# Optimization experiments

Measured on AMD Instinct MI355X. Metric: run time of the kernel, lower is better.

## Reference

```python
import jax, jax.numpy as jnp
import numpy as np

B, N, H, T = 2048, 512, 20, 3

def setup_inputs() -> dict:
    key = jax.random.key(0)
    ks = jax.random.split(key, 10)
    x = jax.random.normal(ks[0], (B, N, H), dtype=jnp.float32)
    # row-stochastic-ish adjacency so time-step iteration stays numerically tame
    A_in = jax.random.uniform(ks[1], (N, N), dtype=jnp.float32) / N
    std = 0.05
    W3w = jax.random.normal(ks[2], (H, 2 * H), dtype=jnp.float32) * std
    W3u = jax.random.normal(ks[3], (H, H), dtype=jnp.float32) * std
    W4w = jax.random.normal(ks[4], (H, 2 * H), dtype=jnp.float32) * std
    W4u = jax.random.normal(ks[5], (H, H), dtype=jnp.float32) * std
    W5w = jax.random.normal(ks[6], (H, 2 * H), dtype=jnp.float32) * std
    W5u = jax.random.normal(ks[7], (H, H), dtype=jnp.float32) * std
    W_out = jax.random.normal(ks[8], (H, 2 * H), dtype=jnp.float32) * std
    b_out = jnp.zeros((H,), dtype=jnp.float32)
    return {"x": x, "A_in": A_in, "W3w": W3w, "W3u": W3u, "W4w": W4w,
            "W4u": W4u, "W5w": W5w, "W5u": W5u, "W_out": W_out, "b_out": b_out}

def reference(x, A_in, W3w, W3u, W4w, W4u, W5w, W5u, W_out, b_out):
    # x: [B, N, H]; A_in: [N, N]; out-matrix is the transpose of in-matrix.
    A_out = A_in.T
    b, n, h = x.shape
    x_flat = x.reshape(b * n, h)              # original 'input' kept for skip-cat
    nodes = x                                  # batch_aog_nodes [B, N, H]
    outputs = []
    for _ in range(T):
        # aggregation: in- and out-neighborhood bmm, then concat -> [B*N, 2H]
        agg_in = jnp.einsum('nm,bmh->bnh', A_in, nodes)
        agg_out = jnp.einsum('nm,bmh->bnh', A_out, nodes)
        av = jnp.concatenate([agg_in, agg_out], axis=-1).reshape(b * n, 2 * h)
        fn = nodes.reshape(b * n, h)
        # GRU-style gates
        zv = jax.nn.sigmoid(av @ W3w.T + fn @ W3u.T)
        rv = jax.nn.sigmoid(av @ W4w.T + fn @ W4u.T)
        hv = jnp.tanh(av @ W5w.T + (rv * fn) @ W5u.T)
        fn = (1.0 - zv) * fn + zv * hv
        nodes = fn.reshape(b, n, h)
        step = jnp.concatenate([fn, x_flat], axis=1) @ W_out.T + b_out
        outputs.append(step.reshape(b, n, -1))
    return jnp.stack(outputs, axis=0)  # [T, B, N, out]; torch returns this as a list per step
```

## Files before the change

kernel.cpp:

```cpp
#include <hip/hip_runtime.h>
#include <stdint.h>

#define B_SZ 2048
#define N_SZ 512
#define H_SZ 20
#define T_STEPS 3

typedef unsigned short u16;
typedef __attribute__((ext_vector_type(8))) short bf8;
typedef __attribute__((ext_vector_type(4))) float f4;

#define MFMA(a, b, c) __builtin_amdgcn_mfma_f32_16x16x32_bf16((a), (b), (c), 0, 0, 0)

__device__ __forceinline__ u16 f2bf(float f) {
    __bf16 h = (__bf16)f;
    union { __bf16 b; u16 u; } v; v.b = h;
    return v.u;
}
__device__ __forceinline__ float bf2f(u16 h) {
    union { uint32_t u; float f; } v; v.u = ((uint32_t)h) << 16;
    return v.f;
}
__device__ __forceinline__ uint32_t pk2(float a, float b) {
    return (uint32_t)f2bf(a) | ((uint32_t)f2bf(b) << 16);
}
__device__ __forceinline__ uint2 pack4(f4 v) {
    uint2 r; r.x = pk2(v[0], v[1]); r.y = pk2(v[2], v[3]); return r;
}
__device__ __forceinline__ int scoff(int c, int f) {
    return c * 64 + (((f >> 3) ^ (c & 7)) << 3) + (f & 7);
}
__device__ __forceinline__ float sigm(float x) { return 1.f / (1.f + __expf(-x)); }


__global__ __launch_bounds__(256)
void prep_fused(const float* __restrict__ x, const float* __restrict__ Wout,
                const float* __restrict__ bout,
                u16* __restrict__ nodes, u16* __restrict__ xo) {
    __shared__ float xt[N_SZ * H_SZ];
    __shared__ float wo2[H_SZ * H_SZ];
    __shared__ float bo[H_SZ];
    int tid = threadIdx.x;
    int b = blockIdx.x;
    const float4* xb4 = (const float4*)(x + (size_t)b * (N_SZ * H_SZ));
    #pragma unroll
    for (int i = 0; i < 10; i++) ((float4*)xt)[i * 256 + tid] = xb4[i * 256 + tid];
    for (int i = tid; i < H_SZ * H_SZ; i += 256)
        wo2[i] = Wout[(i / H_SZ) * 2 * H_SZ + H_SZ + (i % H_SZ)];
    if (tid < H_SZ) bo[tid] = bout[tid];
    __syncthreads();

    u16* nb = nodes + (size_t)b * (N_SZ * H_SZ);
    #pragma unroll
    for (int g0 = 0; g0 < 5; g0++) {
        int g = g0 * 256 + tid;
        int nt = g / 40, r = g - nt * 40;
        int hp = r >> 1, nl0 = (r & 1) * 8;
        union { uint4 v; u16 s[8]; } u;
        #pragma unroll
        for (int j = 0; j < 8; j++) u.s[j] = f2bf(xt[(nt * 16 + nl0 + j) * H_SZ + hp]);
        *(uint4*)&nb[(size_t)g * 8] = u.v;
    }

    u16* ob = xo + (size_t)b * (N_SZ * H_SZ);
    #pragma unroll
    for (int n0 = 0; n0 < 2; n0++) {
        int n = n0 * 256 + tid;
        float xl[H_SZ];
        #pragma unroll
        for (int h = 0; h < H_SZ; h++) xl[h] = xt[n * H_SZ + h];
        #pragma unroll
        for (int q = 0; q < 5; q++) {
            float s[4];
            #pragma unroll
            for (int k = 0; k < 4; k++) {
                int hp = q * 4 + k;
                float acc = bo[hp];
                #pragma unroll
                for (int h = 0; h < H_SZ; h++) acc += xl[h] * wo2[hp * H_SZ + h];
                s[k] = acc;
            }
            uint2 v; v.x = pk2(s[0], s[1]); v.y = pk2(s[2], s[3]);
            *(uint2*)&ob[(size_t)n * H_SZ + q * 4] = v;
        }
    }
}

__global__ void prep_afrag(const float* __restrict__ A, u16* __restrict__ pAT,
                           u16* __restrict__ pA) {
    int idx = blockIdx.x * 256 + threadIdx.x;
    int lane = idx & 63;
    int kt = (idx >> 6) & 15;
    int nt = idx >> 10;
    int n = nt * 16 + (lane & 15);
    int k0 = kt * 32 + (lane >> 4) * 8;
    u16* d1 = pAT + (size_t)idx * 8;
    u16* d2 = pA + (size_t)idx * 8;
    #pragma unroll
    for (int j = 0; j < 8; j++) {
        int m = k0 + j;
        d1[j] = f2bf(A[(size_t)n * N_SZ + m]);
        d2[j] = f2bf(A[(size_t)m * N_SZ + n]);
    }
}

__global__ void prep_wfrag(const float* __restrict__ W3w, const float* __restrict__ W3u,
                           const float* __restrict__ W4w, const float* __restrict__ W4u,
                           const float* __restrict__ W5w, const float* __restrict__ W5u,
                           const float* __restrict__ Wout,
                           u16* __restrict__ wbig, u16* __restrict__ whu, u16* __restrict__ wo1) {
    int t = blockIdx.x * 256 + threadIdx.x;
    int lane = t & 63;
    int l16 = lane & 15, quad = lane >> 4;
    if (t < 768) {
        int kt = (t >> 6) & 1;
        int mt = t >> 7;
        int mrow = mt * 16 + l16;
        int g = mrow >> 5, lr = mrow & 31;
        u16* d = wbig + (size_t)t * 8;
        #pragma unroll
        for (int j = 0; j < 8; j++) {
            int k = kt * 32 + quad * 8 + j;
            float v = 0.f;
            if (lr < 20) {
                if (k < 40) {
                    const float* W = (g == 0) ? W3w : (g == 1) ? W4w : W5w;
                    v = W[lr * 40 + k];
                } else if (k < 60 && g < 2) {
                    const float* U = (g == 0) ? W3u : W4u;
                    v = U[lr * 20 + (k - 40)];
                }
            }
            d[j] = f2bf(v);
        }
    } else if (t < 896) {
        int tt = t - 768;
        int mrow = (tt >> 6) * 16 + l16;
        u16* d = whu + (size_t)tt * 8;
        #pragma unroll
        for (int j = 0; j < 8; j++) {
            int k = quad * 8 + j;
            d[j] = f2bf((mrow < 20 && k < 20) ? W5u[mrow * 20 + k] : 0.f);
        }
    } else {
        int tt = t - 896;
        int mrow = (tt >> 6) * 16 + l16;
        u16* d = wo1 + (size_t)tt * 8;
        #pragma unroll
        for (int j = 0; j < 8; j++) {
            int k = quad * 8 + j;
            d[j] = f2bf((mrow < 20 && k < 20) ? Wout[mrow * 40 + k] : 0.f);
        }
    }
}

__global__ void ws_too_small(float* out) { out[0] = 12345.0f; }

__global__ __launch_bounds__(256, 2)
void step_kernel(const u16* __restrict__ pAT, const u16* __restrict__ pA,
                 const u16* __restrict__ wbig, const u16* __restrict__ whu,
                 const u16* __restrict__ wo1, const u16* __restrict__ xo,
                 u16* __restrict__ nodes, float* __restrict__ out)
{
    __shared__ __align__(16) u16 lds_all[40 * 512 + 4 * 2048];
    u16* Xs = lds_all;
    int tid = threadIdx.x;
    int wv = tid >> 6, lane = tid & 63;
    int l16 = lane & 15, quad = lane >> 4;
    int b0 = blockIdx.x * 2;
    u16* scw = lds_all + 40 * 512 + wv * 2048;

    const u16* nb = nodes + (size_t)b0 * (N_SZ * H_SZ);

    #pragma unroll 1
    for (int t = 0; t < T_STEPS; t++) {
        #pragma unroll
        for (int i = 0; i < 10; i++) {
            int idx = i * 256 + tid;
            uint4 v = *(const uint4*)(nb + (size_t)idx * 8);
            int bs = idx >= 1280 ? 1 : 0;
            int idxb = idx - bs * 1280;
            int nt = idxb / 40;
            int r  = idxb - nt * 40;
            int hp = r >> 1;
            int half = r & 1;
            int row = bs * 20 + hp;
            int mb = nt * 2 + half;
            *(uint4*)&Xs[row * 512 + ((mb ^ (row & 7)) << 3)] = v;
        }
        __syncthreads();

        for (int p = 0; p < 4; p++) {
            int nt0 = wv * 8 + p * 2;

            f4 acc[2][3][2];
            #pragma unroll
            for (int a0 = 0; a0 < 2; a0++)
                #pragma unroll
                for (int a1 = 0; a1 < 3; a1++)
                    #pragma unroll
                    for (int a2 = 0; a2 < 2; a2++)
                        acc[a0][a1][a2] = (f4){0.f, 0.f, 0.f, 0.f};

            for (int kt = 0; kt < 16; kt++) {
                bf8 af[3];
                #pragma unroll
                for (int mt = 0; mt < 3; mt++) {
                    int row = mt * 16 + l16;
                    int kb = (kt * 4 + quad) ^ (row & 7);
                    af[mt] = *(const bf8*)&Xs[row * 512 + kb * 8];
                }
                #pragma unroll
                for (int ntL = 0; ntL < 2; ntL++) {
                    size_t fo = ((size_t)((nt0 + ntL) * 16 + kt) * 64 + lane) * 8;
                    bf8 bi = *(const bf8*)(pAT + fo);
                    bf8 bo = *(const bf8*)(pA + fo);
                    #pragma unroll
                    for (int mt = 0; mt < 3; mt++) {
                        acc[ntL][mt][0] = MFMA(af[mt], bi, acc[ntL][mt][0]);
                        acc[ntL][mt][1] = MFMA(af[mt], bo, acc[ntL][mt][1]);
                    }
                }
            }

            #pragma unroll
            for (int ntL = 0; ntL < 2; ntL++) {
                int nt = nt0 + ntL;
                int nglob = nt * 16 + l16;

                #pragma unroll
                for (int mt = 0; mt < 3; mt++) {
                    if (mt < 2 || quad < 2) {
                        int row0 = mt * 16 + quad * 4;
                        int bs = (row0 >= 20) ? 1 : 0;
                        int h0 = row0 - bs * 20;
                        int c = bs * 16 + l16;
                        *(uint2*)&scw[scoff(c, h0)]      = pack4(acc[ntL][mt][0]);
                        *(uint2*)&scw[scoff(c, 20 + h0)] = pack4(acc[ntL][mt][1]);
                    }
                }
                {
                    int c = lane & 31;
                    int h0 = (lane >> 5) * 10;
                    int bs = c >> 4, nl = c & 15;
                    int m = nt * 16 + nl;
                    int mb = m >> 3, mo = m & 7;
                    u16 fnv[10];
                    #pragma unroll
                    for (int i = 0; i < 10; i++) {
                        int row = bs * 20 + h0 + i;
                        fnv[i] = Xs[row * 512 + ((mb ^ (row & 7)) << 3) + mo];
                    }
                    if (h0 == 0) {
                        uint2 a; a.x = fnv[0] | (fnv[1] << 16); a.y = fnv[2] | (fnv[3] << 16);
                        *(uint2*)&scw[scoff(c, 40)] = a;
                        uint2 b2; b2.x = fnv[4] | (fnv[5] << 16); b2.y = fnv[6] | (fnv[7] << 16);
                        *(uint2*)&scw[scoff(c, 44)] = b2;
                        *(uint32_t*)&scw[scoff(c, 48)] = (uint32_t)fnv[8] | ((uint32_t)fnv[9] << 16);
                    } else {
                        *(uint32_t*)&scw[scoff(c, 50)] = (uint32_t)fnv[0] | ((uint32_t)fnv[1] << 16);
                        uint2 a; a.x = fnv[2] | (fnv[3] << 16); a.y = fnv[4] | (fnv[5] << 16);
                        *(uint2*)&scw[scoff(c, 52)] = a;
                        uint2 b2; b2.x = fnv[6] | (fnv[7] << 16); b2.y = fnv[8] | (fnv[9] << 16);
                        *(uint2*)&scw[scoff(c, 56)] = b2;
                        uint2 z; z.x = 0u; z.y = 0u;
                        *(uint2*)&scw[scoff(c, 60)] = z;
                    }
                }

                f4 g1[6][2];
                #pragma unroll
                for (int a0 = 0; a0 < 6; a0++) { g1[a0][0] = (f4){0,0,0,0}; g1[a0][1] = (f4){0,0,0,0}; }
                #pragma unroll
                for (int kt = 0; kt < 2; kt++) {
                    bf8 bfr[2];
                    #pragma unroll
                    for (int ct = 0; ct < 2; ct++) {
                        int c = ct * 16 + l16;
                        int fb = (kt * 4 + quad) ^ (c & 7);
                        bfr[ct] = *(const bf8*)&scw[c * 64 + fb * 8];
                    }
                    #pragma unroll
                    for (int mt = 0; mt < 6; mt++) {
                        bf8 wf = *(const bf8*)(wbig + ((size_t)(mt * 2 + kt) * 64 + lane) * 8);
                        g1[mt][0] = MFMA(wf, bfr[0], g1[mt][0]);
                        g1[mt][1] = MFMA(wf, bfr[1], g1[mt][1]);
                    }
                }

                float fnr[2][4], fnr2[2][4];
                #pragma unroll
                for (int ct = 0; ct < 2; ct++) {
                    int c = ct * 16 + l16;
                    uint2 fl = *(const uint2*)&scw[scoff(c, 40 + quad * 4)];
                    fnr[ct][0] = bf2f((u16)fl.x);  fnr[ct][1] = bf2f((u16)(fl.x >> 16));
                    fnr[ct][2] = bf2f((u16)fl.y);  fnr[ct][3] = bf2f((u16)(fl.y >> 16));
                    uint2 rp;
                    rp.x = pk2(sigm(g1[2][ct][0]) * fnr[ct][0], sigm(g1[2][ct][1]) * fnr[ct][1]);
                    rp.y = pk2(sigm(g1[2][ct][2]) * fnr[ct][2], sigm(g1[2][ct][3]) * fnr[ct][3]);
                    *(uint2*)&scw[scoff(c, quad * 4)] = rp;
                    if (quad == 0) {
                        uint2 fl2 = *(const uint2*)&scw[scoff(c, 56)];
                        fnr2[ct][0] = bf2f((u16)fl2.x);  fnr2[ct][1] = bf2f((u16)(fl2.x >> 16));
                        fnr2[ct][2] = bf2f((u16)fl2.y);  fnr2[ct][3] = bf2f((u16)(fl2.y >> 16));
                        uint2 rp2;
                        rp2.x = pk2(sigm(g1[3][ct][0]) * fnr2[ct][0], sigm(g1[3][ct][1]) * fnr2[ct][1]);
                        rp2.y = pk2(sigm(g1[3][ct][2]) * fnr2[ct][2], sigm(g1[3][ct][3]) * fnr2[ct][3]);
                        *(uint2*)&scw[scoff(c, 16)] = rp2;
                    }
                }

                f4 hu[2][2];
                hu[0][0] = (f4){0,0,0,0}; hu[0][1] = (f4){0,0,0,0};
                hu[1][0] = (f4){0,0,0,0}; hu[1][1] = (f4){0,0,0,0};
                #pragma unroll
                for (int ct = 0; ct < 2; ct++) {
                    int c = ct * 16 + l16;
                    int fb = quad ^ (c & 7);
                    bf8 bfr = *(const bf8*)&scw[c * 64 + fb * 8];
                    #pragma unroll
                    for (int mt = 0; mt < 2; mt++) {
                        bf8 wf = *(const bf8*)(whu + ((size_t)(mt * 64) + lane) * 8);
                        hu[mt][ct] = MFMA(wf, bfr, hu[mt][ct]);
                    }
                }

                #pragma unroll
                for (int ct = 0; ct < 2; ct++) {
                    int c = ct * 16 + l16;
                    size_t nbase = ((size_t)(b0 + ct) * 32 + nt) * 320 + l16;
                    float w4[4];
                    #pragma unroll
                    for (int r = 0; r < 4; r++) {
                        float z = sigm(g1[0][ct][r]);
                        float hpre = g1[4][ct][r] + hu[0][ct][r];
                        float hv = 2.f / (1.f + __expf(-2.f * hpre)) - 1.f;
                        w4[r] = (1.f - z) * fnr[ct][r] + z * hv;
                    }
                    uint2 wp; wp.x = pk2(w4[0], w4[1]); wp.y = pk2(w4[2], w4[3]);
                    *(uint2*)&scw[scoff(c, quad * 4)] = wp;
                    nodes[nbase + (size_t)(quad * 4 + 0) * 16] = (u16)wp.x;
                    nodes[nbase + (size_t)(quad * 4 + 1) * 16] = (u16)(wp.x >> 16);
                    nodes[nbase + (size_t)(quad * 4 + 2) * 16] = (u16)wp.y;
                    nodes[nbase + (size_t)(quad * 4 + 3) * 16] = (u16)(wp.y >> 16);
                    if (quad == 0) {
                        float w42[4];
                        #pragma unroll
                        for (int r = 0; r < 4; r++) {
                            float z = sigm(g1[1][ct][r]);
                            float hpre = g1[5][ct][r] + hu[1][ct][r];
                            float hv = 2.f / (1.f + __expf(-2.f * hpre)) - 1.f;
                            w42[r] = (1.f - z) * fnr2[ct][r] + z * hv;
                        }
                        uint2 wp2; wp2.x = pk2(w42[0], w42[1]); wp2.y = pk2(w42[2], w42[3]);
                        *(uint2*)&scw[scoff(c, 16)] = wp2;
                        nodes[nbase + (size_t)16 * 16] = (u16)wp2.x;
                        nodes[nbase + (size_t)17 * 16] = (u16)(wp2.x >> 16);
                        nodes[nbase + (size_t)18 * 16] = (u16)wp2.y;
                        nodes[nbase + (size_t)19 * 16] = (u16)(wp2.y >> 16);
                    }
                }

                f4 og[2][2];
                og[0][0] = (f4){0,0,0,0}; og[0][1] = (f4){0,0,0,0};
                og[1][0] = (f4){0,0,0,0}; og[1][1] = (f4){0,0,0,0};
                #pragma unroll
                for (int ct = 0; ct < 2; ct++) {
                    int c = ct * 16 + l16;
                    int fb = quad ^ (c & 7);
                    bf8 bfr = *(const bf8*)&scw[c * 64 + fb * 8];
                    #pragma unroll
                    for (int mt = 0; mt < 2; mt++) {
                        bf8 wf = *(const bf8*)(wo1 + ((size_t)(mt * 64) + lane) * 8);
                        og[mt][ct] = MFMA(wf, bfr, og[mt][ct]);
                    }
                }

                #pragma unroll
                for (int ct = 0; ct < 2; ct++) {
                    int bg = b0 + ct;
                    size_t xob = ((size_t)bg * N_SZ + nglob) * H_SZ;
                    size_t ob = (((size_t)t * B_SZ + bg) * N_SZ + nglob) * H_SZ;
                    {
                        uint2 xp = *(const uint2*)(xo + xob + quad * 4);
                        f4 v;
                        v[0] = og[0][ct][0] + bf2f((u16)xp.x);
                        v[1] = og[0][ct][1] + bf2f((u16)(xp.x >> 16));
                        v[2] = og[0][ct][2] + bf2f((u16)xp.y);
                        v[3] = og[0][ct][3] + bf2f((u16)(xp.y >> 16));
                        *(f4*)(out + ob + quad * 4) = v;
                    }
                    if (quad == 0) {
                        uint2 xp = *(const uint2*)(xo + xob + 16);
                        f4 v;
                        v[0] = og[1][ct][0] + bf2f((u16)xp.x);
                        v[1] = og[1][ct][1] + bf2f((u16)(xp.x >> 16));
                        v[2] = og[1][ct][2] + bf2f((u16)xp.y);
                        v[3] = og[1][ct][3] + bf2f((u16)(xp.y >> 16));
                        *(f4*)(out + ob + 16) = v;
                    }
                }
            }
        }
        if (t < T_STEPS - 1) __syncthreads();
    }
}

#define WS_NODES   0
#define WS_XO      41943040UL
#define WS_PAT     83886080UL
#define WS_PA      84410368UL
#define WS_WBIG    84934656UL
#define WS_WHU     84946944UL
#define WS_WO1     84948992UL
#define WS_NEEDED  84951040UL

extern "C" void kernel_launch(void* const* d_in, const int* in_sizes, int n_in,
                              void* d_out, int out_size, void* d_ws, size_t ws_size,
                              hipStream_t stream) {
    const float* x    = (const float*)d_in[0];
    const float* A    = (const float*)d_in[1];
    const float* W3w  = (const float*)d_in[2];
    const float* W3u  = (const float*)d_in[3];
    const float* W4w  = (const float*)d_in[4];
    const float* W4u  = (const float*)d_in[5];
    const float* W5w  = (const float*)d_in[6];
    const float* W5u  = (const float*)d_in[7];
    const float* Wout = (const float*)d_in[8];
    const float* bout = (const float*)d_in[9];
    float* out = (float*)d_out;

    if (ws_size < WS_NEEDED) {
        ws_too_small<<<1, 1, 0, stream>>>(out);
        return;
    }
    char* ws = (char*)d_ws;
    u16* nodes = (u16*)(ws + WS_NODES);
    u16* xo    = (u16*)(ws + WS_XO);
    u16* pAT   = (u16*)(ws + WS_PAT);
    u16* pA    = (u16*)(ws + WS_PA);
    u16* wbig  = (u16*)(ws + WS_WBIG);
    u16* whu   = (u16*)(ws + WS_WHU);
    u16* wo1   = (u16*)(ws + WS_WO1);

    prep_fused<<<B_SZ, 256, 0, stream>>>(x, Wout, bout, nodes, xo);
    prep_afrag<<<128, 256, 0, stream>>>(A, pAT, pA);
    prep_wfrag<<<4, 256, 0, stream>>>(W3w, W3u, W4w, W4u, W5w, W5u, Wout, wbig, whu, wo1);

    step_kernel<<<B_SZ / 2, 256, 0, stream>>>(pAT, pA, wbig, whu, wo1, xo, nodes, out);
}
```

Measured before the change: 774.1 us.

## Keep recurrent node state in LDS across time steps instead of global round-trips

Each block now loads its node state from global memory once, before the time loop. Updated per-step node values are held in registers and written back into the swizzled LDS tile between two barriers, replacing the global scatter stores and reloads at every step. Several global index calculations also switch from 64-bit to 32-bit arithmetic. This removes per-step global traffic at the cost of extra live registers (sv/sv2 arrays, fully unrolled p loop), which may reduce occupancy or cause spills under the 256x2 launch bounds.

```diff
diff --git a/kernel.cpp b/kernel.cpp
--- a/kernel.cpp
+++ b/kernel.cpp
@@ -160,7 +160,7 @@
 void step_kernel(const u16* __restrict__ pAT, const u16* __restrict__ pA,
                  const u16* __restrict__ wbig, const u16* __restrict__ whu,
                  const u16* __restrict__ wo1, const u16* __restrict__ xo,
-                 u16* __restrict__ nodes, float* __restrict__ out)
+                 const u16* __restrict__ nodes, float* __restrict__ out)
 {
     __shared__ __align__(16) u16 lds_all[40 * 512 + 4 * 2048];
     u16* Xs = lds_all;
@@ -170,10 +170,8 @@
     int b0 = blockIdx.x * 2;
     u16* scw = lds_all + 40 * 512 + wv * 2048;
 
-    const u16* nb = nodes + (size_t)b0 * (N_SZ * H_SZ);
-
-    #pragma unroll 1
-    for (int t = 0; t < T_STEPS; t++) {
+    {
+        const u16* nb = nodes + (size_t)b0 * (N_SZ * H_SZ);
         #pragma unroll
         for (int i = 0; i < 10; i++) {
             int idx = i * 256 + tid;
@@ -188,8 +186,15 @@
             int mb = nt * 2 + half;
             *(uint4*)&Xs[row * 512 + ((mb ^ (row & 7)) << 3)] = v;
         }
-        __syncthreads();
-
+    }
+    __syncthreads();
+
+    #pragma unroll 1
+    for (int t = 0; t < T_STEPS; t++) {
+        uint2 sv[4][2][2];
+        uint2 sv2[4][2][2];
+
+        #pragma unroll
         for (int p = 0; p < 4; p++) {
             int nt0 = wv * 8 + p * 2;
 
@@ -212,7 +217,7 @@
                 }
                 #pragma unroll
                 for (int ntL = 0; ntL < 2; ntL++) {
-                    size_t fo = ((size_t)((nt0 + ntL) * 16 + kt) * 64 + lane) * 8;
+                    uint32_t fo = ((uint32_t)((nt0 + ntL) * 16 + kt) * 64 + (uint32_t)lane) * 8;
                     bf8 bi = *(const bf8*)(pAT + fo);
                     bf8 bo = *(const bf8*)(pA + fo);
                     #pragma unroll
@@ -282,7 +287,7 @@
                     }
                     #pragma unroll
                     for (int mt = 0; mt < 6; mt++) {
-                        bf8 wf = *(const bf8*)(wbig + ((size_t)(mt * 2 + kt) * 64 + lane) * 8);
+                        bf8 wf = *(const bf8*)(wbig + ((uint32_t)(mt * 2 + kt) * 64 + (uint32_t)lane) * 8);
                         g1[mt][0] = MFMA(wf, bfr[0], g1[mt][0]);
                         g1[mt][1] = MFMA(wf, bfr[1], g1[mt][1]);
                     }
@@ -320,7 +325,7 @@
                     bf8 bfr = *(const bf8*)&scw[c * 64 + fb * 8];
                     #pragma unroll
                     for (int mt = 0; mt < 2; mt++) {
-                        bf8 wf = *(const bf8*)(whu + ((size_t)(mt * 64) + lane) * 8);
+                        bf8 wf = *(const bf8*)(whu + ((uint32_t)(mt * 64) + (uint32_t)lane) * 8);
                         hu[mt][ct] = MFMA(wf, bfr, hu[mt][ct]);
                     }
                 }
@@ -328,7 +333,6 @@
                 #pragma unroll
                 for (int ct = 0; ct < 2; ct++) {
                     int c = ct * 16 + l16;
-                    size_t nbase = ((size_t)(b0 + ct) * 32 + nt) * 320 + l16;
                     float w4[4];
                     #pragma unroll
                     for (int r = 0; r < 4; r++) {
@@ -339,10 +343,7 @@
                     }
                     uint2 wp; wp.x = pk2(w4[0], w4[1]); wp.y = pk2(w4[2], w4[3]);
                     *(uint2*)&scw[scoff(c, quad * 4)] = wp;
-                    nodes[nbase + (size_t)(quad * 4 + 0) * 16] = (u16)wp.x;
-                    nodes[nbase + (size_t)(quad * 4 + 1) * 16] = (u16)(wp.x >> 16);
-                    nodes[nbase + (size_t)(quad * 4 + 2) * 16] = (u16)wp.y;
-                    nodes[nbase + (size_t)(quad * 4 + 3) * 16] = (u16)(wp.y >> 16);
+                    sv[p][ntL][ct] = wp;
                     if (quad == 0) {
                         float w42[4];
                         #pragma unroll
@@ -354,10 +355,7 @@
                         }
                         uint2 wp2; wp2.x = pk2(w42[0], w42[1]); wp2.y = pk2(w42[2], w42[3]);
                         *(uint2*)&scw[scoff(c, 16)] = wp2;
-                        nodes[nbase + (size_t)16 * 16] = (u16)wp2.x;
-                        nodes[nbase + (size_t)17 * 16] = (u16)(wp2.x >> 16);
-                        nodes[nbase + (size_t)18 * 16] = (u16)wp2.y;
-                        nodes[nbase + (size_t)19 * 16] = (u16)(wp2.y >> 16);
+                        sv2[p][ntL][ct] = wp2;
                     }
                 }
 
@@ -371,7 +369,7 @@
                     bf8 bfr = *(const bf8*)&scw[c * 64 + fb * 8];
                     #pragma unroll
                     for (int mt = 0; mt < 2; mt++) {
-                        bf8 wf = *(const bf8*)(wo1 + ((size_t)(mt * 64) + lane) * 8);
+                        bf8 wf = *(const bf8*)(wo1 + ((uint32_t)(mt * 64) + (uint32_t)lane) * 8);
                         og[mt][ct] = MFMA(wf, bfr, og[mt][ct]);
                     }
                 }
@@ -402,7 +400,40 @@
                 }
             }
         }
-        if (t < T_STEPS - 1) __syncthreads();
+
+        if (t < T_STEPS - 1) {
+            __syncthreads();
+            #pragma unroll
+            for (int p = 0; p < 4; p++) {
+                #pragma unroll
+                for (int ntL = 0; ntL < 2; ntL++) {
+                    int nt = wv * 8 + p * 2 + ntL;
+                    int m = nt * 16 + l16, mb = m >> 3, mo = m & 7;
+                    #pragma unroll
+                    for (int ct = 0; ct < 2; ct++) {
+                        uint2 wp = sv[p][ntL][ct];
+                        #pragma unroll
+                        for (int r = 0; r < 4; r++) {
+                            int row = ct * 20 + quad * 4 + r;
+                            u16 w = (u16)((r & 1) ? ((r & 2) ? (wp.y >> 16) : (wp.x >> 16))
+                                                  : ((r & 2) ? wp.y : wp.x));
+                            Xs[row * 512 + ((mb ^ (row & 7)) << 3) + mo] = w;
+                        }
+                        if (quad == 0) {
+                            uint2 wp2 = sv2[p][ntL][ct];
+                            #pragma unroll
+                            for (int r = 0; r < 4; r++) {
+                                int row = ct * 20 + 16 + r;
+                                u16 w = (u16)((r & 1) ? ((r & 2) ? (wp2.y >> 16) : (wp2.x >> 16))
+                                                      : ((r & 2) ? wp2.y : wp2.x));
+                                Xs[row * 512 + ((mb ^ (row & 7)) << 3) + mo] = w;
+                            }
+                        }
+                    }
+                }
+            }
+            __syncthreads();
+        }
     }
 }
 
```

Measured after the change: 2.223 ms. 187% more time.
